# Kernel optimization log

Measured on AMD Instinct MI355X. Metric: run time of the kernel, lower is better.

## Reference

```python
import jax, jax.numpy as jnp
import numpy as np

B, H, W, C = 8, 256, 256, 32
WIN = 8
HEADS = 2
DH = C // HEADS          # 16
HIDDEN = 128             # mlp_ratio * C
N = WIN * WIN            # 64 tokens per window


def _rel_index(win):
    # standard Swin relative position index, computed once (static int constant)
    coords = np.stack(np.meshgrid(np.arange(win), np.arange(win), indexing='ij'))  # [2,w,w]
    coords = coords.reshape(2, -1)                                                  # [2,N]
    rel = (coords[:, :, None] - coords[:, None, :]).transpose(1, 2, 0)              # [N,N,2]
    rel[:, :, 0] += win - 1
    rel[:, :, 1] += win - 1
    rel[:, :, 0] *= 2 * win - 1
    return jnp.asarray(rel.sum(-1))                                                 # [N,N]

REL_IDX = _rel_index(WIN)


def setup_inputs() -> dict:
    key = jax.random.key(0)
    ks = jax.random.split(key, 10)
    rn = lambda k, s: jax.random.normal(k, s, jnp.float32) * 0.02
    return {
        'x': jax.random.normal(ks[0], (B, H * W, C), jnp.float32),
        'norm1_g': jnp.ones((C,), jnp.float32), 'norm1_b': jnp.zeros((C,), jnp.float32),
        'wq': rn(ks[1], (C, C)), 'bq': jnp.zeros((C,), jnp.float32),
        'wkv': rn(ks[2], (C, 2 * C)), 'bkv': jnp.zeros((2 * C,), jnp.float32),
        'wo': rn(ks[3], (C, C)), 'bo': jnp.zeros((C,), jnp.float32),
        'rel_bias': rn(ks[4], ((2 * WIN - 1) ** 2, HEADS)),
        'norm2_g': jnp.ones((C,), jnp.float32), 'norm2_b': jnp.zeros((C,), jnp.float32),
        'w1': rn(ks[5], (C, HIDDEN)), 'b1': jnp.zeros((HIDDEN,), jnp.float32),
        'dw': rn(ks[6], (HIDDEN, 1, 3, 3)), 'dwb': jnp.zeros((HIDDEN,), jnp.float32),
        'w2': rn(ks[7], (HIDDEN, C)), 'b2': jnp.zeros((C,), jnp.float32),
    }


def _ln(x, g, b):
    mu = x.mean(-1, keepdims=True)
    var = x.var(-1, keepdims=True)
    return (x - mu) / jnp.sqrt(var + 1e-5) * g + b


def _gelu(x):
    return jax.nn.gelu(x, approximate=False)  # torch nn.GELU is exact erf


def reference(x, norm1_g, norm1_b, wq, bq, wkv, bkv, wo, bo, rel_bias,
              norm2_g, norm2_b, w1, b1, dw, dwb, w2, b2):
    shortcut = x                                              # [B, HW, C]
    xn = _ln(x, norm1_g, norm1_b).reshape(B, H, W, C)
    # window partition -> [B*nW, N, C]
    xw = (xn.reshape(B, H // WIN, WIN, W // WIN, WIN, C)
            .transpose(0, 1, 3, 2, 4, 5)
            .reshape(-1, N, C))
    # linear qkv projection
    q = (xw @ wq + bq).reshape(-1, N, HEADS, DH).transpose(0, 2, 1, 3)      # [B_,h,N,d]
    kv = (xw @ wkv + bkv).reshape(-1, N, 2, HEADS, DH).transpose(2, 0, 3, 1, 4)
    k, v = kv[0], kv[1]
    scale = DH ** -0.5
    attn = jnp.einsum('bhnd,bhmd->bhnm', q * scale, k)                      # [B_,h,N,N]
    bias = rel_bias[REL_IDX].transpose(2, 0, 1)                             # [h,N,N]
    attn = jax.nn.softmax(attn + bias[None], axis=-1)
    out = jnp.einsum('bhnm,bhmd->bhnd', attn, v).transpose(0, 2, 1, 3).reshape(-1, N, C)
    out = out @ wo + bo
    # window reverse -> [B, HW, C]
    out = (out.reshape(B, H // WIN, W // WIN, WIN, WIN, C)
              .transpose(0, 1, 3, 2, 4, 5)
              .reshape(B, H * W, C))
    x = shortcut + out
    # LeFF: linear -> dwconv3x3 over full HxW map -> linear
    y = _ln(x, norm2_g, norm2_b)
    y = _gelu(y @ w1 + b1)                                                  # [B,HW,HIDDEN]
    y = y.reshape(B, H, W, HIDDEN).transpose(0, 3, 1, 2)                    # NCHW
    y = jax.lax.conv_general_dilated(
        y, dw, window_strides=(1, 1), padding='SAME',
        dimension_numbers=('NCHW', 'OIHW', 'NCHW'), feature_group_count=HIDDEN)
    y = _gelu(y + dwb[None, :, None, None])
    y = y.transpose(0, 2, 3, 1).reshape(B, H * W, HIDDEN)
    y = y @ w2 + b2
    return x + y
```

## Files before the change

kernel.cpp:

```cpp
#include <hip/hip_runtime.h>
#include <hip/hip_bf16.h>
#include <math.h>

#define IMG   256
#define HWTOK 65536
#define CH    32

typedef __attribute__((ext_vector_type(8))) _Float16 half8v;
typedef __attribute__((ext_vector_type(2))) _Float16 half2v;
typedef __attribute__((ext_vector_type(4))) float floatx4;

__device__ __forceinline__ unsigned short f2h(float f) {
    _Float16 h = (_Float16)f;
    return __builtin_bit_cast(unsigned short, h);
}
__device__ __forceinline__ float h2f(unsigned short u) {
    return (float)__builtin_bit_cast(_Float16, u);
}
__device__ __forceinline__ unsigned packh2(float a, float b) {
    return (unsigned)f2h(a) | ((unsigned)f2h(b) << 16);
}

__device__ __forceinline__ half2v gelu2v(half2v v) {
    const half2v hi = (half2v)(_Float16)( 2.0f);
    const half2v lo = (half2v)(_Float16)(-2.0f);
    const half2v vc = __builtin_elementwise_min(__builtin_elementwise_max(v, lo), hi);
    const half2v s  = vc * vc;
    half2v p = s * (half2v)(_Float16)(-1.18726e-3f) + (half2v)(_Float16)(9.97356e-3f);
    p = s * p + (half2v)(_Float16)(-6.64904e-2f);
    p = s * p + (half2v)(_Float16)( 3.989423e-1f);
    return v * (vc * p + (half2v)(_Float16)(0.5f));
}

__global__ __launch_bounds__(256) void attn_kernel(
    const float* __restrict__ x,
    const float* __restrict__ n1g, const float* __restrict__ n1b,
    const float* __restrict__ wq,  const float* __restrict__ bq,
    const float* __restrict__ wkv, const float* __restrict__ bkv,
    const float* __restrict__ wo,  const float* __restrict__ bo,
    const float* __restrict__ relb,
    float* __restrict__ x1)
{
    struct Win {
        union {
            unsigned short xn[64][40];
            unsigned short P[2][64][72];
            unsigned short O[64][40];
        } u;
        unsigned short Q[64][40];
        unsigned short K[64][56];
        unsigned short VT[2][16][72];
    };
    __shared__ Win W[2];
    __shared__ unsigned short bias16[2][228];
    __shared__ float denom[2][2][64];

    const int tid = threadIdx.x;
    const int wv  = tid >> 6;
    const int w   = wv >> 1;
    const int h   = wv & 1;
    const int l   = tid & 63;
    const int lm  = l & 15, lq = l >> 4;
    Win& S = W[w];

    const int win = blockIdx.x * 2 + w;
    const int b   = win >> 10;
    const int wh  = (win >> 5) & 31, ww = win & 31;
    const size_t wbase = ((size_t)b * HWTOK + (wh * 8) * IMG + ww * 8) * CH;

    const float LOG2E = 1.4426950408889634f;
    const float QSC   = 0.25f * LOG2E;

    half8v bwq, bwk, bwv, bwo0, bwo1;
    {
        const int lq8 = lq * 8;
        #pragma unroll
        for (int i = 0; i < 8; ++i) {
            bwq[i]  = (_Float16)(wq[(lq8 + i) * 32 + h * 16 + lm] * QSC);
            bwk[i]  = (_Float16)wkv[(lq8 + i) * 64 + h * 16 + lm];
            bwv[i]  = (_Float16)wkv[(lq8 + i) * 64 + 32 + h * 16 + lm];
            bwo0[i] = (_Float16)wo [(lq8 + i) * 32 + lm];
            bwo1[i] = (_Float16)wo [(lq8 + i) * 32 + 16 + lm];
        }
    }

    if (tid < 128) {
        const int sw = tid >> 6, st = tid & 63;
        Win& SS = W[sw];
        const int swin = blockIdx.x * 2 + sw;
        const int sb = swin >> 10, swh = (swin >> 5) & 31, sww = swin & 31;
        const size_t sbase = ((size_t)sb * HWTOK
                            + (swh * 8 + (st >> 3)) * IMG + sww * 8 + (st & 7)) * CH;
        const float4* xp = (const float4*)(x + sbase);
        float xr[32];
        float mu = 0.f;
        #pragma unroll
        for (int i = 0; i < 8; ++i) {
            const float4 v = xp[i];
            xr[i*4+0]=v.x; xr[i*4+1]=v.y; xr[i*4+2]=v.z; xr[i*4+3]=v.w;
            mu += v.x + v.y + v.z + v.w;
        }
        mu *= (1.f / 32.f);
        float var = 0.f;
        #pragma unroll
        for (int c = 0; c < 32; ++c) { const float d = xr[c] - mu; var += d * d; }
        const float inv = rsqrtf(var * (1.f / 32.f) + 1e-5f);
        unsigned int pk[16];
        #pragma unroll
        for (int j = 0; j < 16; ++j)
            pk[j] = packh2((xr[2*j]   - mu) * inv * n1g[2*j]   + n1b[2*j],
                           (xr[2*j+1] - mu) * inv * n1g[2*j+1] + n1b[2*j+1]);
        uint4* dst = (uint4*)&SS.u.xn[st][0];
        #pragma unroll
        for (int j = 0; j < 4; ++j) dst[j] = *(uint4*)&pk[j * 4];
        const uint4 z = {0u, 0u, 0u, 0u};
        *(uint4*)&SS.K[st][16] = z;
        *(uint4*)&SS.K[st][24] = z;
    } else {
        const int t2 = tid - 128;
        for (int i = t2; i < 450; i += 128) {
            const int hh = (i >= 225), r = i - hh * 225;
            bias16[hh][r] = f2h(relb[r * 2 + hh] * LOG2E);
        }
    }
    __syncthreads();

    const float bqv = bq[h*16 + lm] * QSC;
    const float bkv_ = bkv[h*16 + lm];
    const float bvv = bkv[32 + h*16 + lm];
    const floatx4 cq = {bqv, bqv, bqv, bqv};
    const floatx4 ck = {bkv_, bkv_, bkv_, bkv_};
    const floatx4 cv = {bvv, bvv, bvv, bvv};
    const floatx4 zero = {0.f, 0.f, 0.f, 0.f};

    #pragma unroll
    for (int mt = 0; mt < 4; ++mt) {
        const half8v a = *(const half8v*)&S.u.xn[mt*16 + lm][lq*8];
        const floatx4 dq = __builtin_amdgcn_mfma_f32_16x16x32_f16(a, bwq, cq, 0,0,0);
        const floatx4 dk = __builtin_amdgcn_mfma_f32_16x16x32_f16(a, bwk, ck, 0,0,0);
        const floatx4 dv = __builtin_amdgcn_mfma_f32_16x16x32_f16(a, bwv, cv, 0,0,0);
        const int r0 = mt*16 + lq*4;
        #pragma unroll
        for (int r = 0; r < 4; ++r) {
            S.Q[r0 + r][h*16 + lm] = f2h(dq[r]);
            S.K[r0 + r][h*32 + lm] = f2h(dk[r]);
        }
        uint2 vv;
        vv.x = packh2(dv[0], dv[1]);
        vv.y = packh2(dv[2], dv[3]);
        *(uint2*)&S.VT[h][lm][r0] = vv;
    }
    __syncthreads();

    half8v ak[4], bqf[4];
    #pragma unroll
    for (int mt = 0; mt < 4; ++mt)
        ak[mt] = *(const half8v*)&S.K[mt*16 + lm][h*16 + lq*8];
    #pragma unroll
    for (int nt = 0; nt < 4; ++nt)
        bqf[nt] = *(const half8v*)&S.Q[nt*16 + lm][lq*8];

    const int cc0 = (lm >> 3) * 15 + (lm & 7);
    const int cml = 15 * (lq >> 1) + 4 * (lq & 1);

    #pragma unroll
    for (int nt = 0; nt < 4; ++nt) {
        float sum = 0.f;
        const int base_nt = 30*nt + cc0 + 112 - cml;
        #pragma unroll
        for (int mt = 0; mt < 4; ++mt) {
            const floatx4 d = __builtin_amdgcn_mfma_f32_16x16x32_f16(ak[mt], bqf[nt], zero, 0,0,0);
            const int ib = base_nt - 30*mt;
            const float e0 = exp2f(d[0] + h2f(bias16[h][ib]));
            const float e1 = exp2f(d[1] + h2f(bias16[h][ib - 1]));
            const float e2 = exp2f(d[2] + h2f(bias16[h][ib - 2]));
            const float e3 = exp2f(d[3] + h2f(bias16[h][ib - 3]));
            sum += (e0 + e1) + (e2 + e3);
            uint2 pw;
            pw.x = packh2(e0, e1);
            pw.y = packh2(e2, e3);
            *(uint2*)&S.u.P[h][nt*16 + lm][mt*16 + lq*4] = pw;
        }
        sum += __shfl_xor(sum, 16);
        sum += __shfl_xor(sum, 32);
        if (l < 16) denom[w][h][nt*16 + l] = __frcp_rn(sum);
    }

    const half8v bva = *(const half8v*)&S.VT[h][lm][lq*8];
    const half8v bvb = *(const half8v*)&S.VT[h][lm][32 + lq*8];
    float oreg[16];
    #pragma unroll
    for (int mt = 0; mt < 4; ++mt) {
        const half8v ap0 = *(const half8v*)&S.u.P[h][mt*16 + lm][lq*8];
        const half8v ap1 = *(const half8v*)&S.u.P[h][mt*16 + lm][32 + lq*8];
        floatx4 ov = __builtin_amdgcn_mfma_f32_16x16x32_f16(ap0, bva, zero, 0,0,0);
        ov         = __builtin_amdgcn_mfma_f32_16x16x32_f16(ap1, bvb, ov,   0,0,0);
        const float4 dn = *(const float4*)&denom[w][h][mt*16 + lq*4];
        oreg[mt*4+0] = ov[0] * dn.x;
        oreg[mt*4+1] = ov[1] * dn.y;
        oreg[mt*4+2] = ov[2] * dn.z;
        oreg[mt*4+3] = ov[3] * dn.w;
    }
    __syncthreads();

    #pragma unroll
    for (int mt = 0; mt < 4; ++mt)
        #pragma unroll
        for (int r = 0; r < 4; ++r)
            S.u.O[mt*16 + lq*4 + r][h*16 + lm] = f2h(oreg[mt*4 + r]);
    __syncthreads();

    const float bo0 = bo[lm], bo1 = bo[16 + lm];
    const floatx4 co0 = {bo0, bo0, bo0, bo0};
    const floatx4 co1 = {bo1, bo1, bo1, bo1};
    #pragma unroll
    for (int mi = 0; mi < 2; ++mi) {
        const int mt = 2*h + mi;
        const half8v aO = *(const half8v*)&S.u.O[mt*16 + lm][lq*8];
        const floatx4 d0 = __builtin_amdgcn_mfma_f32_16x16x32_f16(aO, bwo0, co0, 0,0,0);
        const floatx4 d1 = __builtin_amdgcn_mfma_f32_16x16x32_f16(aO, bwo1, co1, 0,0,0);
        #pragma unroll
        for (int r = 0; r < 4; ++r) {
            const int t = mt*16 + lq*4 + r;
            const size_t g = wbase + (size_t)((t >> 3) * IMG + (t & 7)) * CH;
            x1[g + lm]      = x[g + lm]      + d0[r];
            x1[g + 16 + lm] = x[g + 16 + lm] + d1[r];
        }
    }
}

__global__ __launch_bounds__(256, 3) void leff_kernel(
    const float* __restrict__ x1,
    const float* __restrict__ n2g, const float* __restrict__ n2b,
    const float* __restrict__ w1,  const float* __restrict__ b1,
    const float* __restrict__ dw,  const float* __restrict__ dwb,
    const float* __restrict__ w2,  const float* __restrict__ b2,
    float* __restrict__ out)
{
    union SharedU {
        struct { unsigned short xnA[112][40]; unsigned short w1T[128][40]; } p1;
        struct { unsigned short glA[64][136]; unsigned short w2T[32][136]; } p3;
    };
    __shared__ __align__(16) SharedU u;
    __shared__ __align__(16) unsigned short hid[100][132];

    const int blk = blockIdx.x;
    const int b = blk >> 10, tyb = (blk >> 5) & 31, txb = blk & 31;
    const int y0 = tyb * 8, x0 = txb * 8;
    const int tid = threadIdx.x;
    const int wv = tid >> 6;
    const int l  = tid & 63;
    const int lm = l & 15;
    const int lq = l >> 4;
    const bool edge = (tyb == 0) | (tyb == 31) | (txb == 0) | (txb == 31);

    if (tid < 200) {
        const int px = tid >> 1, half = tid & 1;
        const int hy = px / 10, hx = px % 10;
        const int iy = y0 + hy - 1, ix = x0 + hx - 1;
        const bool inb = (iy >= 0 && iy < IMG && ix >= 0 && ix < IMG);
        unsigned int pk[8];
        if (inb) {
            const size_t base = ((size_t)b * HWTOK + iy * IMG + ix) * CH + half * 16;
            const float4* xp = (const float4*)(x1 + base);
            float v[16];
            float s = 0.f;
            #pragma unroll
            for (int i = 0; i < 4; ++i) {
                const float4 t = xp[i];
                v[i*4+0]=t.x; v[i*4+1]=t.y; v[i*4+2]=t.z; v[i*4+3]=t.w;
                s += t.x + t.y + t.z + t.w;
            }
            const float mu = (s + __shfl_xor(s, 1)) * (1.f / 32.f);
            float q = 0.f;
            #pragma unroll
            for (int c = 0; c < 16; ++c) { const float d = v[c]-mu; q += d*d; }
            const float var = q + __shfl_xor(q, 1);
            const float inv = rsqrtf(var * (1.f/32.f) + 1e-5f);
            #pragma unroll
            for (int j = 0; j < 8; ++j) {
                const int c = half*16 + 2*j;
                pk[j] = packh2((v[2*j]   - mu) * inv * n2g[c]   + n2b[c],
                               (v[2*j+1] - mu) * inv * n2g[c+1] + n2b[c+1]);
            }
        } else {
            #pragma unroll
            for (int j = 0; j < 8; ++j) pk[j] = 0u;
        }
        uint4* dst = (uint4*)&u.p1.xnA[px][half * 16];
        dst[0] = *(uint4*)&pk[0];
        dst[1] = *(uint4*)&pk[4];
    } else if (tid < 248) {
        const int t2 = tid - 200;
        const uint4 z = {0u,0u,0u,0u};
        *(uint4*)&u.p1.xnA[100 + (t2 >> 2)][(t2 & 3) * 8] = z;
    }
    #pragma unroll
    for (int i = 0; i < 2; ++i) {
        const int o = tid + i * 256;
        const int row = o & 127, cq = o >> 7;
        const int bl = row >> 5, wi = row & 31;
        const int j = bl * 32 + ((wi & 15) << 1) + (wi >> 4);
        const int k0 = cq * 8;
        unsigned int pk4[4];
        #pragma unroll
        for (int jj = 0; jj < 4; ++jj)
            pk4[jj] = packh2(w1[(k0 + 2*jj) * 128 + j], w1[(k0 + 2*jj + 1) * 128 + j]);
        *(uint4*)&u.p1.w1T[row][k0] = *(uint4*)&pk4[0];
    }
    __syncthreads();

    {
        const int c0 = wv * 32 + 2 * lm;
        const half8v bf0 = *(const half8v*)&u.p1.w1T[wv * 32 + lm][lq * 8];
        const half8v bf1 = *(const half8v*)&u.p1.w1T[wv * 32 + 16 + lm][lq * 8];
        const float bias0 = b1[c0], bias1 = b1[c0 + 1];
        const floatx4 cb0 = {bias0, bias0, bias0, bias0};
        const floatx4 cb1 = {bias1, bias1, bias1, bias1};
        for (int mt = 0; mt < 7; ++mt) {
            const half8v af = *(const half8v*)&u.p1.xnA[mt * 16 + lm][lq * 8];
            floatx4 a0 = __builtin_amdgcn_mfma_f32_16x16x32_f16(af, bf0, cb0, 0, 0, 0);
            floatx4 a1 = __builtin_amdgcn_mfma_f32_16x16x32_f16(af, bf1, cb1, 0, 0, 0);
            #pragma unroll
            for (int r = 0; r < 4; ++r) {
                const int p = mt * 16 + lq * 4 + r;
                if (mt < 6 || p < 100) {
                    half2v hv;
                    hv.x = (_Float16)a0[r];
                    hv.y = (_Float16)a1[r];
                    half2v g = gelu2v(hv);
                    unsigned int bits = __builtin_bit_cast(unsigned int, g);
                    if (edge) {
                        const int hy = (p * 205) >> 11;
                        const int hx = p - hy * 10;
                        const int iy = y0 + hy - 1, ix = x0 + hx - 1;
                        const bool inb = (iy >= 0) & (iy < IMG) & (ix >= 0) & (ix < IMG);
                        if (!inb) bits = 0u;
                    }
                    *(unsigned int*)&hid[p][c0] = bits;
                }
            }
        }
    }
    __syncthreads();

    {
        const int jq = tid & 31, pg = tid >> 5;
        const int j0 = 4 * jq;
        half2v dwa[9], dwc[9];
        #pragma unroll
        for (int t = 0; t < 9; ++t) {
            dwa[t].x = (_Float16)dw[(j0    ) * 9 + t];
            dwa[t].y = (_Float16)dw[(j0 + 1) * 9 + t];
            dwc[t].x = (_Float16)dw[(j0 + 2) * 9 + t];
            dwc[t].y = (_Float16)dw[(j0 + 3) * 9 + t];
        }
        half2v acca[8], accc[8];
        {
            half2v dba, dbc;
            dba.x = (_Float16)dwb[j0];     dba.y = (_Float16)dwb[j0 + 1];
            dbc.x = (_Float16)dwb[j0 + 2]; dbc.y = (_Float16)dwb[j0 + 3];
            #pragma unroll
            for (int i = 0; i < 8; ++i) { acca[i] = dba; accc[i] = dbc; }
        }
        #pragma unroll
        for (int ky = 0; ky < 3; ++ky) {
            uint2 rr[10];
            #pragma unroll
            for (int cx = 0; cx < 10; ++cx)
                rr[cx] = *(const uint2*)&hid[(pg + ky) * 10 + cx][j0];
            #pragma unroll
            for (int i = 0; i < 8; ++i)
                #pragma unroll
                for (int kx = 0; kx < 3; ++kx) {
                    acca[i] = __builtin_bit_cast(half2v, rr[i + kx].x) * dwa[ky*3+kx] + acca[i];
                    accc[i] = __builtin_bit_cast(half2v, rr[i + kx].y) * dwc[ky*3+kx] + accc[i];
                }
        }
        #pragma unroll
        for (int i = 0; i < 8; ++i) {
            const half2v ga = gelu2v(acca[i]);
            const half2v gc = gelu2v(accc[i]);
            uint2 ow;
            ow.x = __builtin_bit_cast(unsigned int, ga);
            ow.y = __builtin_bit_cast(unsigned int, gc);
            *(uint2*)&u.p3.glA[pg * 8 + i][j0] = ow;
        }
        #pragma unroll
        for (int i = 0; i < 2; ++i) {
            const int o = tid + i * 256;
            const int c = o & 31, kq = o >> 5;
            const int k0 = kq * 8;
            unsigned int pk4[4];
            #pragma unroll
            for (int jj = 0; jj < 4; ++jj)
                pk4[jj] = packh2(w2[(k0 + 2*jj) * 32 + c], w2[(k0 + 2*jj + 1) * 32 + c]);
            *(uint4*)&u.p3.w2T[c][k0] = *(uint4*)&pk4[0];
        }
    }
    __syncthreads();

    {
        #pragma unroll
        for (int t = 0; t < 2; ++t) {
            const int idx = 2 * wv + t;
            const int mt = idx >> 1, nt = idx & 1;
            const int c = nt * 16 + lm;
            const float bias = b2[c];
            floatx4 acc = {bias, bias, bias, bias};
            #pragma unroll
            for (int kc = 0; kc < 4; ++kc) {
                const half8v a  = *(const half8v*)&u.p3.glA[mt * 16 + lm][kc * 32 + lq * 8];
                const half8v bb = *(const half8v*)&u.p3.w2T[nt * 16 + lm][kc * 32 + lq * 8];
                acc = __builtin_amdgcn_mfma_f32_16x16x32_f16(a, bb, acc, 0, 0, 0);
            }
            #pragma unroll
            for (int r = 0; r < 4; ++r) {
                const int p = mt * 16 + lq * 4 + r;
                const int iy = y0 + (p >> 3), ix = x0 + (p & 7);
                const size_t g = ((size_t)b * HWTOK + iy * IMG + ix) * CH + c;
                out[g] = x1[g] + acc[r];
            }
        }
    }
}

extern "C" void kernel_launch(void* const* d_in, const int* in_sizes, int n_in,
                              void* d_out, int out_size, void* d_ws, size_t ws_size,
                              hipStream_t stream)
{
    const float* x    = (const float*)d_in[0];
    const float* n1g  = (const float*)d_in[1];
    const float* n1b  = (const float*)d_in[2];
    const float* wq   = (const float*)d_in[3];
    const float* bq   = (const float*)d_in[4];
    const float* wkv  = (const float*)d_in[5];
    const float* bkv  = (const float*)d_in[6];
    const float* wo   = (const float*)d_in[7];
    const float* bo   = (const float*)d_in[8];
    const float* relb = (const float*)d_in[9];
    const float* n2g  = (const float*)d_in[10];
    const float* n2b  = (const float*)d_in[11];
    const float* w1   = (const float*)d_in[12];
    const float* b1   = (const float*)d_in[13];
    const float* dw   = (const float*)d_in[14];
    const float* dwb  = (const float*)d_in[15];
    const float* w2   = (const float*)d_in[16];
    const float* b2   = (const float*)d_in[17];

    float* out = (float*)d_out;
    float* x1  = (float*)d_ws;

    attn_kernel<<<4096, 256, 0, stream>>>(x, n1g, n1b, wq, bq, wkv, bkv,
                                          wo, bo, relb, x1);
    leff_kernel<<<8192, 256, 0, stream>>>(x1, n2g, n2b, w1, b1, dw, dwb,
                                          w2, b2, out);
}
```

Measured before the change: 154.8 us.

## Prepack fp16 MLP weights once in attention kernel, load LeFF weights into registers

One extra block appended to the attention launch converts w1 and w2 to fp16 once, in the transposed and permuted MFMA layout, and writes them to workspace. The LeFF kernel then reads its B-operand fragments straight from global memory into registers. This removes the per-block weight transpose and pack and the LDS staging for w1T and w2T, which shrinks shared memory and drops the hid row padding. The costs are an extra __syncthreads before glA is written, since glA now aliases xnA, more registers held for the w2 fragments, and a reliance on stream order so the packed weights are ready before LeFF starts.

New measurement: 158.8 us. 2.6% more time.

```diff
diff --git a/kernel.cpp b/kernel.cpp
--- a/kernel.cpp
+++ b/kernel.cpp
@@ -39,8 +39,24 @@
     const float* __restrict__ wkv, const float* __restrict__ bkv,
     const float* __restrict__ wo,  const float* __restrict__ bo,
     const float* __restrict__ relb,
+    const float* __restrict__ w1,  const float* __restrict__ w2,
+    unsigned short* __restrict__ w1p, unsigned short* __restrict__ w2p,
     float* __restrict__ x1)
 {
+    if (blockIdx.x >= 4096) {
+        #pragma unroll
+        for (int i = 0; i < 16; ++i) {
+            const int t = threadIdx.x + i * 256;
+            const int row = t >> 5, k = t & 31;
+            const int bl = row >> 5, wi = row & 31;
+            const int j = bl * 32 + ((wi & 15) << 1) + (wi >> 4);
+            w1p[t] = f2h(w1[k * 128 + j]);
+            const int n = t >> 7, kk = t & 127;
+            w2p[t] = f2h(w2[kk * 32 + n]);
+        }
+        return;
+    }
+
     struct Win {
         union {
             unsigned short xn[64][40];
@@ -229,20 +245,22 @@
     }
 }
 
-__global__ __launch_bounds__(256, 3) void leff_kernel(
+__global__ __launch_bounds__(256, 3) void leff_kernel_gw(
     const float* __restrict__ x1,
     const float* __restrict__ n2g, const float* __restrict__ n2b,
-    const float* __restrict__ w1,  const float* __restrict__ b1,
+    const float* __restrict__ b1,
     const float* __restrict__ dw,  const float* __restrict__ dwb,
-    const float* __restrict__ w2,  const float* __restrict__ b2,
+    const float* __restrict__ b2,
+    const unsigned short* __restrict__ w1p,
+    const unsigned short* __restrict__ w2p,
     float* __restrict__ out)
 {
     union SharedU {
-        struct { unsigned short xnA[112][40]; unsigned short w1T[128][40]; } p1;
-        struct { unsigned short glA[64][136]; unsigned short w2T[32][136]; } p3;
+        unsigned short xnA[112][40];
+        unsigned short glA[64][132];
     };
     __shared__ __align__(16) SharedU u;
-    __shared__ __align__(16) unsigned short hid[100][132];
+    __shared__ __align__(16) unsigned short hid[100][128];
 
     const int blk = blockIdx.x;
     const int b = blk >> 10, tyb = (blk >> 5) & 31, txb = blk & 31;
@@ -253,6 +271,15 @@
     const int lm = l & 15;
     const int lq = l >> 4;
     const bool edge = (tyb == 0) | (tyb == 31) | (txb == 0) | (txb == 31);
+
+    const half8v bf0 = *(const half8v*)&w1p[(wv * 32 + lm) * 32 + lq * 8];
+    const half8v bf1 = *(const half8v*)&w1p[(wv * 32 + 16 + lm) * 32 + lq * 8];
+    half8v w2f[2][4];
+    #pragma unroll
+    for (int nt = 0; nt < 2; ++nt)
+        #pragma unroll
+        for (int kc = 0; kc < 4; ++kc)
+            w2f[nt][kc] = *(const half8v*)&w2p[(nt*16 + lm) * 128 + kc*32 + lq*8];
 
     if (tid < 200) {
         const int px = tid >> 1, half = tid & 1;
@@ -287,38 +314,23 @@
             #pragma unroll
             for (int j = 0; j < 8; ++j) pk[j] = 0u;
         }
-        uint4* dst = (uint4*)&u.p1.xnA[px][half * 16];
+        uint4* dst = (uint4*)&u.xnA[px][half * 16];
         dst[0] = *(uint4*)&pk[0];
         dst[1] = *(uint4*)&pk[4];
     } else if (tid < 248) {
         const int t2 = tid - 200;
         const uint4 z = {0u,0u,0u,0u};
-        *(uint4*)&u.p1.xnA[100 + (t2 >> 2)][(t2 & 3) * 8] = z;
-    }
-    #pragma unroll
-    for (int i = 0; i < 2; ++i) {
-        const int o = tid + i * 256;
-        const int row = o & 127, cq = o >> 7;
-        const int bl = row >> 5, wi = row & 31;
-        const int j = bl * 32 + ((wi & 15) << 1) + (wi >> 4);
-        const int k0 = cq * 8;
-        unsigned int pk4[4];
-        #pragma unroll
-        for (int jj = 0; jj < 4; ++jj)
-            pk4[jj] = packh2(w1[(k0 + 2*jj) * 128 + j], w1[(k0 + 2*jj + 1) * 128 + j]);
-        *(uint4*)&u.p1.w1T[row][k0] = *(uint4*)&pk4[0];
+        *(uint4*)&u.xnA[100 + (t2 >> 2)][(t2 & 3) * 8] = z;
     }
     __syncthreads();
 
     {
         const int c0 = wv * 32 + 2 * lm;
-        const half8v bf0 = *(const half8v*)&u.p1.w1T[wv * 32 + lm][lq * 8];
-        const half8v bf1 = *(const half8v*)&u.p1.w1T[wv * 32 + 16 + lm][lq * 8];
         const float bias0 = b1[c0], bias1 = b1[c0 + 1];
         const floatx4 cb0 = {bias0, bias0, bias0, bias0};
         const floatx4 cb1 = {bias1, bias1, bias1, bias1};
         for (int mt = 0; mt < 7; ++mt) {
-            const half8v af = *(const half8v*)&u.p1.xnA[mt * 16 + lm][lq * 8];
+            const half8v af = *(const half8v*)&u.xnA[mt * 16 + lm][lq * 8];
             floatx4 a0 = __builtin_amdgcn_mfma_f32_16x16x32_f16(af, bf0, cb0, 0, 0, 0);
             floatx4 a1 = __builtin_amdgcn_mfma_f32_16x16x32_f16(af, bf1, cb1, 0, 0, 0);
             #pragma unroll
@@ -377,6 +389,7 @@
                     accc[i] = __builtin_bit_cast(half2v, rr[i + kx].y) * dwc[ky*3+kx] + accc[i];
                 }
         }
+        __syncthreads();
         #pragma unroll
         for (int i = 0; i < 8; ++i) {
             const half2v ga = gelu2v(acca[i]);
@@ -384,35 +397,22 @@
             uint2 ow;
             ow.x = __builtin_bit_cast(unsigned int, ga);
             ow.y = __builtin_bit_cast(unsigned int, gc);
-            *(uint2*)&u.p3.glA[pg * 8 + i][j0] = ow;
-        }
-        #pragma unroll
-        for (int i = 0; i < 2; ++i) {
-            const int o = tid + i * 256;
-            const int c = o & 31, kq = o >> 5;
-            const int k0 = kq * 8;
-            unsigned int pk4[4];
-            #pragma unroll
-            for (int jj = 0; jj < 4; ++jj)
-                pk4[jj] = packh2(w2[(k0 + 2*jj) * 32 + c], w2[(k0 + 2*jj + 1) * 32 + c]);
-            *(uint4*)&u.p3.w2T[c][k0] = *(uint4*)&pk4[0];
+            *(uint2*)&u.glA[pg * 8 + i][j0] = ow;
         }
     }
     __syncthreads();
 
     {
         #pragma unroll
-        for (int t = 0; t < 2; ++t) {
-            const int idx = 2 * wv + t;
-            const int mt = idx >> 1, nt = idx & 1;
+        for (int nt = 0; nt < 2; ++nt) {
+            const int mt = wv;
             const int c = nt * 16 + lm;
             const float bias = b2[c];
             floatx4 acc = {bias, bias, bias, bias};
             #pragma unroll
             for (int kc = 0; kc < 4; ++kc) {
-                const half8v a  = *(const half8v*)&u.p3.glA[mt * 16 + lm][kc * 32 + lq * 8];
-                const half8v bb = *(const half8v*)&u.p3.w2T[nt * 16 + lm][kc * 32 + lq * 8];
-                acc = __builtin_amdgcn_mfma_f32_16x16x32_f16(a, bb, acc, 0, 0, 0);
+                const half8v a = *(const half8v*)&u.glA[mt * 16 + lm][kc * 32 + lq * 8];
+                acc = __builtin_amdgcn_mfma_f32_16x16x32_f16(a, w2f[nt][kc], acc, 0, 0, 0);
             }
             #pragma unroll
             for (int r = 0; r < 4; ++r) {
@@ -450,9 +450,12 @@
 
     float* out = (float*)d_out;
     float* x1  = (float*)d_ws;
-
-    attn_kernel<<<4096, 256, 0, stream>>>(x, n1g, n1b, wq, bq, wkv, bkv,
-                                          wo, bo, relb, x1);
-    leff_kernel<<<8192, 256, 0, stream>>>(x1, n2g, n2b, w1, b1, dw, dwb,
-                                          w2, b2, out);
-}
+    const size_t X1_BYTES = (size_t)8 * HWTOK * CH * 4;
+    unsigned short* w1p = (unsigned short*)((char*)d_ws + X1_BYTES);
+    unsigned short* w2p = w1p + 4096;
+
+    attn_kernel<<<4097, 256, 0, stream>>>(x, n1g, n1b, wq, bq, wkv, bkv,
+                                          wo, bo, relb, w1, w2, w1p, w2p, x1);
+    leff_kernel_gw<<<8192, 256, 0, stream>>>(x1, n2g, n2b, b1, dw, dwb,
+                                             b2, w1p, w2p, out);
+}
```
